# Kernel optimization log

Hardware: AMD Instinct MI355X
Metric: run time of the kernel (lower is better)

The kernel has to match this reference:

```python
import jax, jax.numpy as jnp
import numpy as np

L, D, DM, H, FF = 2048, 32, 1024, 16, 4096
DH = DM // H  # 64
SCALE = float(np.sqrt(DH))


def layernorm(x, g, b, eps=1e-5):
    mu = jnp.mean(x, axis=-1, keepdims=True)
    var = jnp.mean(jnp.square(x - mu), axis=-1, keepdims=True)
    return (x - mu) * jax.lax.rsqrt(var + eps) * g + b


def setup_inputs() -> dict:
    key = jax.random.key(0)
    ks = jax.random.split(key, 8)
    p = lambda k, shp: jax.random.normal(k, shp, jnp.float32) * 0.02
    return {
        "src": jax.random.normal(ks[0], (L, DM), jnp.float32),
        "target": jax.random.normal(ks[1], (L, D, DM), jnp.float32),
        "attn_mask": jnp.zeros((L, D), jnp.float32),
        "Wq": p(ks[2], (DM, DM)), "bq": jnp.zeros((DM,), jnp.float32),
        "Wk": p(ks[3], (DM, DM)), "bk": jnp.zeros((DM,), jnp.float32),
        "Wv": p(ks[4], (DM, DM)), "bv": jnp.zeros((DM,), jnp.float32),
        "W1": p(ks[5], (DM, FF)), "b1": jnp.zeros((FF,), jnp.float32),
        "W2": p(ks[6], (FF, DM)), "b2": jnp.zeros((DM,), jnp.float32),
        "g1": jnp.ones((DM,), jnp.float32), "beta1": jnp.zeros((DM,), jnp.float32),
        "g2": jnp.ones((DM,), jnp.float32), "beta2": jnp.zeros((DM,), jnp.float32),
    }


def reference(src, target, attn_mask, Wq, bq, Wk, bk, Wv, bv,
              W1, b1, W2, b2, g1, beta1, g2, beta2):
    # projections: src (L, DM), target (L, D, DM)
    q = (src @ Wq + bq).reshape(L, H, DH)            # (L, H, DH)
    k = (target @ Wk + bk).reshape(L, D, H, DH)       # (L, D, H, DH)
    v = (target @ Wv + bv).reshape(L, D, H, DH)
    # per-position attention over the D candidates: scores (H, L, D)
    scores = jnp.einsum('lhd,lkhd->hlk', q, k) / SCALE
    scores = scores + attn_mask[None, :, :]
    probs = jax.nn.softmax(scores, axis=-1)
    ctx = jnp.einsum('hlk,lkhd->lhd', probs, v).reshape(L, DM)
    x = layernorm(src + ctx, g1, beta1)
    ff = jax.nn.gelu(x @ W1 + b1, approximate=False) @ W2 + b2
    return layernorm(x + ff, g2, beta2)
```

## Files before the change

kernel.cpp:

```cpp
#include <hip/hip_runtime.h>
#include <hip/hip_bf16.h>

#define L  2048
#define D  32
#define DM 1024
#define H  16
#define DH 64
#define FF 4096

typedef unsigned short u16;
typedef __attribute__((ext_vector_type(8))) short bf16x8;
typedef __attribute__((ext_vector_type(4))) float f32x4;
typedef __attribute__((ext_vector_type(4))) unsigned int u32x4;
typedef __attribute__((ext_vector_type(8))) unsigned short u16x8;
typedef __attribute__((ext_vector_type(4))) unsigned short u16x4;

static __device__ __forceinline__ u16 f2bf(float f) {
    union { __hip_bfloat16 b; u16 u; } cv;
    cv.b = __float2bfloat16(f);
    return cv.u;
}
static __device__ __forceinline__ void gll16(const u16* gsrc, u16* ldst) {
    __builtin_amdgcn_global_load_lds(
        (const __attribute__((address_space(1))) unsigned int*)gsrc,
        (__attribute__((address_space(3))) unsigned int*)ldst, 16, 0, 0);
}

__global__ __launch_bounds__(256) void prep_all(
    const float* __restrict__ src, u16* __restrict__ osrc,
    const float* __restrict__ Wk,  u16* __restrict__ oWk,
    const float* __restrict__ Wq,  u16* __restrict__ oWq,
    const float* __restrict__ Wv,  u16* __restrict__ oWv,
    const float* __restrict__ W1,  u16* __restrict__ oW1,
    const float* __restrict__ W2,  u16* __restrict__ oW2)
{
    const int b = blockIdx.x, t = threadIdx.x;
    if (b >= 10240) {
        const int i = (b - 10240) * 256 + t;
        const int na4 = (L * DM) / 4;
        const float* in;  u16* out;  int j;
        if (i < na4) { in = src; out = osrc; j = i; }
        else         { in = Wk;  out = oWk;  j = i - na4; }
        const float4 v = reinterpret_cast<const float4*>(in)[j];
        u16x4 o = { f2bf(v.x), f2bf(v.y), f2bf(v.z), f2bf(v.w) };
        *reinterpret_cast<u16x4*>(out + (long)j * 4) = o;
        return;
    }
    __shared__ float tile[32][33];
    const float* in; u16* out; int R, C, bx, by;
    if (b < 1024)      { in = Wq; out = oWq; R = DM; C = DM; int bb = b;        bx = (bb & 31) * 32;  by = (bb >> 5) * 32; }
    else if (b < 2048) { in = Wv; out = oWv; R = DM; C = DM; int bb = b - 1024; bx = (bb & 31) * 32;  by = (bb >> 5) * 32; }
    else if (b < 6144) { in = W1; out = oW1; R = DM; C = FF; int bb = b - 2048; bx = (bb & 127) * 32; by = (bb >> 7) * 32; }
    else               { in = W2; out = oW2; R = FF; C = DM; int bb = b - 6144; bx = (bb & 31) * 32;  by = (bb >> 5) * 32; }
    const int tx = t & 31, ty = t >> 5;
    #pragma unroll
    for (int i = 0; i < 32; i += 8)
        tile[ty + i][tx] = in[(long)(by + ty + i) * C + bx + tx];
    __syncthreads();
    #pragma unroll
    for (int i = 0; i < 32; i += 8)
        out[(long)(bx + ty + i) * R + by + tx] = f2bf(tile[tx][ty + i]);
}

template<int EPI, int BN, int PIPE>
__global__ __launch_bounds__(256) void gemm128(
    const u16* __restrict__ A, int lda, long aZ,
    const u16* __restrict__ Bt, int ldb, long bZ,
    void* __restrict__ Cv, int ldc, long cZ,
    const float* __restrict__ bias, int biasZ, int K)
{
    constexpr int NI = BN / 32;
    constexpr int ASZ = 128 * 64, BSZ = BN * 64;
    __shared__ u16 As[(PIPE ? 2 : 1) * ASZ];
    __shared__ u16 Bs[(PIPE ? 2 : 1) * BSZ];
    const int t = threadIdx.x, lane = t & 63, w = t >> 6;
    const int z = blockIdx.z;
    const int nxy = gridDim.x * gridDim.y;
    int fid = blockIdx.y * gridDim.x + blockIdx.x;
    const int q8 = nxy >> 3;
    fid = (fid & 7) * q8 + (fid >> 3);
    const int bx = fid % gridDim.x, by = fid / gridDim.x;
    const int mBase = by * 128, nBase = bx * BN;
    const u16* Ab = A + (long)z * aZ;
    const u16* Bb = Bt + (long)z * bZ;
    const int wr = w >> 1, wc = w & 1;
    const int sr = lane >> 3, sg = lane & 7, sswz = sg ^ sr;
    f32x4 acc[4][NI];
    #pragma unroll
    for (int mi = 0; mi < 4; ++mi)
        #pragma unroll
        for (int ni = 0; ni < NI; ++ni) acc[mi][ni] = (f32x4){0.f, 0.f, 0.f, 0.f};

    auto STAGE = [&](int buf, int k0) {
        u16* Ad = As + buf * ASZ;
        u16* Bd = Bs + buf * BSZ;
        #pragma unroll
        for (int i = 0; i < 4; ++i) {
            const int r = w * 32 + i * 8 + sr;
            gll16(&Ab[(long)(mBase + r) * lda + k0 + sswz * 8], &Ad[r * 64 + sg * 8]);
        }
        #pragma unroll
        for (int i = 0; i < NI; ++i) {
            const int r = w * (BN / 4) + i * 8 + sr;
            gll16(&Bb[(long)(nBase + r) * ldb + k0 + sswz * 8], &Bd[r * 64 + sg * 8]);
        }
    };

    if (PIPE) { STAGE(0, 0); }
    int cur = 0;
    for (int k0 = 0; k0 < K; k0 += 64) {
        if (!PIPE) {
            STAGE(0, k0);
            __syncthreads();
        } else {
            __syncthreads();
            if (k0 + 64 < K) STAGE(cur ^ 1, k0 + 64);
        }
        const u16* Ar = As + cur * ASZ;
        const u16* Br = Bs + cur * BSZ;
        __builtin_amdgcn_s_setprio(1);
        #pragma unroll
        for (int ks = 0; ks < 2; ++ks) {
            bf16x8 aF[4], bF[NI];
            #pragma unroll
            for (int mi = 0; mi < 4; ++mi) {
                const int rr = wr * 64 + mi * 16 + (lane & 15);
                aF[mi] = *reinterpret_cast<const bf16x8*>(
                    &Ar[rr * 64 + ((ks * 4 + (lane >> 4)) ^ (rr & 7)) * 8]);
            }
            #pragma unroll
            for (int ni = 0; ni < NI; ++ni) {
                const int rr = wc * (BN / 2) + ni * 16 + (lane & 15);
                bF[ni] = *reinterpret_cast<const bf16x8*>(
                    &Br[rr * 64 + ((ks * 4 + (lane >> 4)) ^ (rr & 7)) * 8]);
            }
            #pragma unroll
            for (int mi = 0; mi < 4; ++mi)
                #pragma unroll
                for (int ni = 0; ni < NI; ++ni)
                    acc[mi][ni] = __builtin_amdgcn_mfma_f32_16x16x32_bf16(
                        aF[mi], bF[ni], acc[mi][ni], 0, 0, 0);
        }
        __builtin_amdgcn_s_setprio(0);
        if (!PIPE) __syncthreads();
        if (PIPE) cur ^= 1;
    }
    const int rb = mBase + wr * 64 + ((lane >> 4) << 2);
    const int cb = nBase + wc * (BN / 2) + (lane & 15);
    #pragma unroll
    for (int mi = 0; mi < 4; ++mi) {
        #pragma unroll
        for (int ni = 0; ni < NI; ++ni) {
            const int col = cb + ni * 16;
            const float badd = bias ? bias[(long)z * biasZ + col] : 0.f;
            #pragma unroll
            for (int i = 0; i < 4; ++i) {
                float v = acc[mi][ni][i] + badd;
                if (EPI == 2) v = 0.5f * v * (1.f + erff(v * 0.70710678118654752f));
                const long off = (long)z * cZ + (long)(rb + mi * 16 + i) * ldc + col;
                if (EPI == 1) reinterpret_cast<float*>(Cv)[off] = v;
                else          reinterpret_cast<u16*>(Cv)[off]  = f2bf(v);
            }
        }
    }
}

#define NLV5 8
__global__ __launch_bounds__(512, 2) void attn_v5(
    const u16* __restrict__ qk,
    const float* __restrict__ target,
    const float* __restrict__ mask,
    u16* __restrict__ tw)
{
    extern __shared__ u16 smem[];
    u16*   tgtS0 = smem;
    u16*   tgtS1 = smem + D * DM;
    f32x4* red   = (f32x4*)(smem + 2 * D * DM);

    const int t = threadIdx.x, lane = t & 63, w = t >> 6;
    const int g = lane >> 4, hm = lane & 15;
    const int l0 = blockIdx.x * NLV5;

    float4 pf[16];
    bf16x8 qc[2][4];
    {
        const float* tl = target + (long)l0 * (D * DM);
        #pragma unroll
        for (int it = 0; it < 16; ++it)
            pf[it] = reinterpret_cast<const float4*>(tl)[it * 512 + t];
        #pragma unroll
        for (int it = 0; it < 16; ++it) {
            const int i = it * 512 + t;
            const int d = i >> 8, mm = (i & 255) * 4, cc = mm ^ ((d & 15) << 3);
            u16x4 o = { f2bf(pf[it].x), f2bf(pf[it].y), f2bf(pf[it].z), f2bf(pf[it].w) };
            *reinterpret_cast<u16x4*>(&tgtS0[d * DM + cc]) = o;
        }
        const float* tn = target + (long)(l0 + 1) * (D * DM);
        #pragma unroll
        for (int it = 0; it < 16; ++it)
            pf[it] = reinterpret_cast<const float4*>(tn)[it * 512 + t];
        const u16* qb = qk + (long)l0 * (H * DM) + hm * DM + w * 128 + g * 8;
        #pragma unroll
        for (int ks = 0; ks < 4; ++ks)
            qc[0][ks] = *reinterpret_cast<const bf16x8*>(&qb[ks * 32]);
    }
    __syncthreads();

    #pragma unroll
    for (int li = 0; li < NLV5; ++li) {
        const int l = l0 + li;
        const int cur = li & 1, nxt = cur ^ 1;
        u16* curS = cur ? tgtS1 : tgtS0;
        u16* nxtS = cur ? tgtS0 : tgtS1;

        const float* mrow = mask + (long)l * D;
        float mk[8];
        #pragma unroll
        for (int r = 0; r < 4; ++r) { mk[r] = mrow[4 * g + r]; mk[4 + r] = mrow[16 + 4 * g + r]; }

        if (li < NLV5 - 1) {
            #pragma unroll
            for (int it = 0; it < 16; ++it) {
                const int i = it * 512 + t;
                const int d = i >> 8, mm = (i & 255) * 4, cc = mm ^ ((d & 15) << 3);
                u16x4 o = { f2bf(pf[it].x), f2bf(pf[it].y), f2bf(pf[it].z), f2bf(pf[it].w) };
                *reinterpret_cast<u16x4*>(&nxtS[d * DM + cc]) = o;
            }
            if (li < NLV5 - 2) {
                const float* tn = target + (long)(l + 2) * (D * DM);
                #pragma unroll
                for (int it = 0; it < 16; ++it)
                    pf[it] = reinterpret_cast<const float4*>(tn)[it * 512 + t];
            }
            const u16* qn = qk + (long)(l + 1) * (H * DM) + hm * DM + w * 128 + g * 8;
            #pragma unroll
            for (int ks = 0; ks < 4; ++ks)
                qc[nxt][ks] = *reinterpret_cast<const bf16x8*>(&qn[ks * 32]);
        }

        f32x4 a0 = {0.f, 0.f, 0.f, 0.f}, a1 = {0.f, 0.f, 0.f, 0.f};
        const int swz = hm << 3;
        #pragma unroll
        for (int ks = 0; ks < 4; ++ks) {
            const int mcol = w * 128 + ks * 32 + g * 8;
            const bf16x8 x0 = *reinterpret_cast<const bf16x8*>(&curS[hm * DM + (mcol ^ swz)]);
            const bf16x8 x1 = *reinterpret_cast<const bf16x8*>(&curS[(16 + hm) * DM + (mcol ^ swz)]);
            a0 = __builtin_amdgcn_mfma_f32_16x16x32_bf16(x0, qc[cur][ks], a0, 0, 0, 0);
            a1 = __builtin_amdgcn_mfma_f32_16x16x32_bf16(x1, qc[cur][ks], a1, 0, 0, 0);
        }
        red[(w * 2 + 0) * 64 + lane] = a0;
        red[(w * 2 + 1) * 64 + lane] = a1;
        __syncthreads();

        f32x4 s0 = red[lane], s1 = red[64 + lane];
        #pragma unroll
        for (int ww = 1; ww < 8; ++ww) {
            s0 += red[(ww * 2 + 0) * 64 + lane];
            s1 += red[(ww * 2 + 1) * 64 + lane];
        }

        float sc[8];
        #pragma unroll
        for (int r = 0; r < 4; ++r) {
            sc[r]     = s0[r] * 0.125f + mk[r];
            sc[4 + r] = s1[r] * 0.125f + mk[4 + r];
        }
        float mx = sc[0];
        #pragma unroll
        for (int r = 1; r < 8; ++r) mx = fmaxf(mx, sc[r]);
        mx = fmaxf(mx, __shfl_xor(mx, 16));
        mx = fmaxf(mx, __shfl_xor(mx, 32));
        float sum = 0.f;
        #pragma unroll
        for (int r = 0; r < 8; ++r) { sc[r] = __expf(sc[r] - mx); sum += sc[r]; }
        sum += __shfl_xor(sum, 16);
        sum += __shfl_xor(sum, 32);
        const float pinv = 1.0f / sum;
        bf16x8 pfrag;
        #pragma unroll
        for (int r = 0; r < 8; ++r) pfrag[r] = (short)f2bf(sc[r] * pinv);

        u16* twl = tw + (long)l * (H * DM);
        const f32x4 zero = {0.f, 0.f, 0.f, 0.f};
        #pragma unroll
        for (int i = 0; i < 8; ++i) {
            const int mg = w * 8 + i;
            const int m = mg * 16 + hm;
            bf16x8 af;
            #pragma unroll
            for (int j = 0; j < 4; ++j) {
                const int d0 = 4 * g + j;
                const int d1 = 16 + 4 * g + j;
                af[j]     = (short)curS[d0 * DM + (m ^ (d0 << 3))];
                af[4 + j] = (short)curS[d1 * DM + (m ^ (d0 << 3))];
            }
            const f32x4 c = __builtin_amdgcn_mfma_f32_16x16x32_bf16(af, pfrag, zero, 0, 0, 0);
            u16x4 o = { f2bf(c[0]), f2bf(c[1]), f2bf(c[2]), f2bf(c[3]) };
            *reinterpret_cast<u16x4*>(&twl[hm * DM + mg * 16 + 4 * g]) = o;
        }
        __syncthreads();
    }
}

__global__ __launch_bounds__(256) void ln_fuse(
    const float* __restrict__ a, const float* __restrict__ zb, int nz, long zstride,
    const float* __restrict__ bvec,
    const float* __restrict__ g, const float* __restrict__ be,
    float* __restrict__ o32, u16* __restrict__ o16)
{
    const int l = blockIdx.x, t = threadIdx.x;
    __shared__ float S[4], SS[4];
    __shared__ float stats[2];
    const float4 va = reinterpret_cast<const float4*>(a + (long)l * DM)[t];
    float v[4] = { va.x, va.y, va.z, va.w };
    for (int zi = 0; zi < nz; ++zi) {
        const float4 q = reinterpret_cast<const float4*>(zb + (long)zi * zstride + (long)l * DM)[t];
        v[0] += q.x; v[1] += q.y; v[2] += q.z; v[3] += q.w;
    }
    if (bvec) {
        const float4 vv = reinterpret_cast<const float4*>(bvec)[t];
        v[0] += vv.x; v[1] += vv.y; v[2] += vv.z; v[3] += vv.w;
    }
    float s  = v[0] + v[1] + v[2] + v[3];
    float ss = v[0]*v[0] + v[1]*v[1] + v[2]*v[2] + v[3]*v[3];
    #pragma unroll
    for (int off = 32; off; off >>= 1) { s += __shfl_down(s, off); ss += __shfl_down(ss, off); }
    if ((t & 63) == 0) { S[t >> 6] = s; SS[t >> 6] = ss; }
    __syncthreads();
    if (t == 0) {
        const float St  = S[0] + S[1] + S[2] + S[3];
        const float SSt = SS[0] + SS[1] + SS[2] + SS[3];
        const float mu  = St * (1.f / DM);
        const float var = fmaxf(SSt * (1.f / DM) - mu * mu, 0.f);
        stats[0] = mu;
        stats[1] = rsqrtf(var + 1e-5f);
    }
    __syncthreads();
    const float mu = stats[0], rs = stats[1];
    const int c0 = t * 4;
    float ov[4];
    #pragma unroll
    for (int j = 0; j < 4; ++j) ov[j] = (v[j] - mu) * rs * g[c0 + j] + be[c0 + j];
    float4 o; o.x = ov[0]; o.y = ov[1]; o.z = ov[2]; o.w = ov[3];
    reinterpret_cast<float4*>(o32 + (long)l * DM)[t] = o;
    if (o16) {
        u16x4 q = { f2bf(ov[0]), f2bf(ov[1]), f2bf(ov[2]), f2bf(ov[3]) };
        *reinterpret_cast<u16x4*>(o16 + (long)l * DM + c0) = q;
    }
}

extern "C" void kernel_launch(void* const* d_in, const int* in_sizes, int n_in,
                              void* d_out, int out_size, void* d_ws, size_t ws_size,
                              hipStream_t stream)
{
    const float* src    = (const float*)d_in[0];
    const float* target = (const float*)d_in[1];
    const float* amask  = (const float*)d_in[2];
    const float* Wq = (const float*)d_in[3];
    const float* bq = (const float*)d_in[4];
    const float* Wk = (const float*)d_in[5];
    const float* Wv = (const float*)d_in[7];
    const float* bv = (const float*)d_in[8];
    const float* W1 = (const float*)d_in[9];
    const float* b1 = (const float*)d_in[10];
    const float* W2 = (const float*)d_in[11];
    const float* b2 = (const float*)d_in[12];
    const float* g1  = (const float*)d_in[13];
    const float* be1 = (const float*)d_in[14];
    const float* g2  = (const float*)d_in[15];
    const float* be2 = (const float*)d_in[16];

    char* ws = (char*)d_ws;
    const size_t MB = (size_t)1 << 20;
    u16*   src16 = (u16*)  (ws +  0 * MB);
    u16*   Wk16  = (u16*)  (ws +  4 * MB);
    u16*   WqT   = (u16*)  (ws +  6 * MB);
    u16*   WvT   = (u16*)  (ws +  8 * MB);
    u16*   W1T   = (u16*)  (ws + 10 * MB);
    u16*   W2T   = (u16*)  (ws + 18 * MB);
    u16*   Q16   = (u16*)  (ws + 26 * MB);
    u16*   qk16  = (u16*)  (ws + 30 * MB);
    u16*   Y16   = (u16*)  (ws + 30 * MB);
    float* ctx32 = (float*)(ws + 54 * MB);
    float* x32   = (float*)(ws + 62 * MB);
    u16*   x16   = (u16*)  (ws + 70 * MB);
    u16*   tw16  = (u16*)  (ws + 94 * MB);
    float* Z32   = (float*)(ws + 94 * MB);

    prep_all<<<13312, 256, 0, stream>>>(src, src16, Wk, Wk16,
                                        Wq, WqT, Wv, WvT, W1, W1T, W2, W2T);

    gemm128<0, 64, 1><<<dim3(DM / 64, L / 128, 1), 256, 0, stream>>>(
        src16, DM, 0, WqT, DM, 0, Q16, DM, 0, bq, 0, DM);
    gemm128<0, 128, 0><<<dim3(DM / 128, L / 128, H), 256, 0, stream>>>(
        Q16, DM, DH, Wk16, DM, DH, qk16, H * DM, DM, nullptr, 0, DH);

    (void)hipFuncSetAttribute(reinterpret_cast<const void*>(&attn_v5),
                              hipFuncAttributeMaxDynamicSharedMemorySize, 144 * 1024);
    attn_v5<<<L / NLV5, 512, 144 * 1024, stream>>>(qk16, target, amask, tw16);

    gemm128<1, 64, 1><<<dim3(1, L / 128, H), 256, 0, stream>>>(
        tw16, H * DM, DM, WvT, DM, (long)DH * DM, ctx32, DM, DH, bv, DH, DM);
    ln_fuse<<<L, 256, 0, stream>>>(src, ctx32, 1, 0, nullptr, g1, be1, x32, x16);
    gemm128<2, 128, 1><<<dim3(FF / 128, L / 128, 1), 256, 0, stream>>>(
        x16, DM, 0, W1T, DM, 0, Y16, FF, 0, b1, 0, DM);
    gemm128<1, 128, 1><<<dim3(DM / 128, L / 128, 4), 256, 0, stream>>>(
        Y16, FF, 1024, W2T, FF, 1024, Z32, DM, (long)L * DM, nullptr, 0, 1024);
    ln_fuse<<<L, 256, 0, stream>>>(x32, Z32, 4, (long)L * DM, b2, g2, be2, (float*)d_out, nullptr);
}
```

Before: 242.7 us.

## Compute attention scores redundantly per wave to drop cross-wave LDS reduction

In the attention kernel, each wave now computes the full 1024-long score dot product itself. Before, each wave covered a 128-column slice and the partial scores were reduced through shared memory. This removes the reduction buffer, one barrier per position and the register double-buffering of q, which is now loaded directly from global memory inside the loop. The cost is eight times more score MFMAs and eight times more shared and global reads for the score phase, since every wave repeats the same work. Shared memory per block drops from 144 KB to 128 KB.

```diff
diff --git a/kernel.cpp b/kernel.cpp
--- a/kernel.cpp
+++ b/kernel.cpp
@@ -165,24 +165,19 @@
     }
 }
 
-#define NLV5 8
-__global__ __launch_bounds__(512, 2) void attn_v5(
+#define NLV6 8
+__global__ __launch_bounds__(512, 2) void attn_v6(
     const u16* __restrict__ qk,
     const float* __restrict__ target,
     const float* __restrict__ mask,
     u16* __restrict__ tw)
 {
     extern __shared__ u16 smem[];
-    u16*   tgtS0 = smem;
-    u16*   tgtS1 = smem + D * DM;
-    f32x4* red   = (f32x4*)(smem + 2 * D * DM);
-
     const int t = threadIdx.x, lane = t & 63, w = t >> 6;
     const int g = lane >> 4, hm = lane & 15;
-    const int l0 = blockIdx.x * NLV5;
+    const int l0 = blockIdx.x * NLV6;
 
     float4 pf[16];
-    bf16x8 qc[2][4];
     {
         const float* tl = target + (long)l0 * (D * DM);
         #pragma unroll
@@ -193,32 +188,22 @@
             const int i = it * 512 + t;
             const int d = i >> 8, mm = (i & 255) * 4, cc = mm ^ ((d & 15) << 3);
             u16x4 o = { f2bf(pf[it].x), f2bf(pf[it].y), f2bf(pf[it].z), f2bf(pf[it].w) };
-            *reinterpret_cast<u16x4*>(&tgtS0[d * DM + cc]) = o;
+            *reinterpret_cast<u16x4*>(&smem[d * DM + cc]) = o;
         }
         const float* tn = target + (long)(l0 + 1) * (D * DM);
         #pragma unroll
         for (int it = 0; it < 16; ++it)
             pf[it] = reinterpret_cast<const float4*>(tn)[it * 512 + t];
-        const u16* qb = qk + (long)l0 * (H * DM) + hm * DM + w * 128 + g * 8;
-        #pragma unroll
-        for (int ks = 0; ks < 4; ++ks)
-            qc[0][ks] = *reinterpret_cast<const bf16x8*>(&qb[ks * 32]);
-    }
-    __syncthreads();
-
-    #pragma unroll
-    for (int li = 0; li < NLV5; ++li) {
+    }
+
+    #pragma unroll
+    for (int li = 0; li < NLV6; ++li) {
         const int l = l0 + li;
-        const int cur = li & 1, nxt = cur ^ 1;
-        u16* curS = cur ? tgtS1 : tgtS0;
-        u16* nxtS = cur ? tgtS0 : tgtS1;
-
-        const float* mrow = mask + (long)l * D;
-        float mk[8];
-        #pragma unroll
-        for (int r = 0; r < 4; ++r) { mk[r] = mrow[4 * g + r]; mk[4 + r] = mrow[16 + 4 * g + r]; }
-
-        if (li < NLV5 - 1) {
+        u16* curS = (li & 1) ? smem + D * DM : smem;
+        u16* nxtS = (li & 1) ? smem : smem + D * DM;
+        __syncthreads();
+
+        if (li < NLV6 - 1) {
             #pragma unroll
             for (int it = 0; it < 16; ++it) {
                 const int i = it * 512 + t;
@@ -226,44 +211,37 @@
                 u16x4 o = { f2bf(pf[it].x), f2bf(pf[it].y), f2bf(pf[it].z), f2bf(pf[it].w) };
                 *reinterpret_cast<u16x4*>(&nxtS[d * DM + cc]) = o;
             }
-            if (li < NLV5 - 2) {
+            if (li < NLV6 - 2) {
                 const float* tn = target + (long)(l + 2) * (D * DM);
                 #pragma unroll
                 for (int it = 0; it < 16; ++it)
                     pf[it] = reinterpret_cast<const float4*>(tn)[it * 512 + t];
             }
-            const u16* qn = qk + (long)(l + 1) * (H * DM) + hm * DM + w * 128 + g * 8;
-            #pragma unroll
-            for (int ks = 0; ks < 4; ++ks)
-                qc[nxt][ks] = *reinterpret_cast<const bf16x8*>(&qn[ks * 32]);
-        }
-
-        f32x4 a0 = {0.f, 0.f, 0.f, 0.f}, a1 = {0.f, 0.f, 0.f, 0.f};
+        }
+
+        const float* mrow = mask + (long)l * D;
+        float mk[8];
+        #pragma unroll
+        for (int r = 0; r < 4; ++r) { mk[r] = mrow[4 * g + r]; mk[4 + r] = mrow[16 + 4 * g + r]; }
+
+        f32x4 acc0 = {0.f, 0.f, 0.f, 0.f}, acc1 = {0.f, 0.f, 0.f, 0.f};
+        const u16* qrow = qk + (long)l * (H * DM) + hm * DM;
         const int swz = hm << 3;
-        #pragma unroll
-        for (int ks = 0; ks < 4; ++ks) {
-            const int mcol = w * 128 + ks * 32 + g * 8;
+        #pragma unroll 4
+        for (int ks = 0; ks < 32; ++ks) {
+            const int mcol = ks * 32 + g * 8;
+            const bf16x8 yf = *reinterpret_cast<const bf16x8*>(&qrow[mcol]);
             const bf16x8 x0 = *reinterpret_cast<const bf16x8*>(&curS[hm * DM + (mcol ^ swz)]);
             const bf16x8 x1 = *reinterpret_cast<const bf16x8*>(&curS[(16 + hm) * DM + (mcol ^ swz)]);
-            a0 = __builtin_amdgcn_mfma_f32_16x16x32_bf16(x0, qc[cur][ks], a0, 0, 0, 0);
-            a1 = __builtin_amdgcn_mfma_f32_16x16x32_bf16(x1, qc[cur][ks], a1, 0, 0, 0);
-        }
-        red[(w * 2 + 0) * 64 + lane] = a0;
-        red[(w * 2 + 1) * 64 + lane] = a1;
-        __syncthreads();
-
-        f32x4 s0 = red[lane], s1 = red[64 + lane];
-        #pragma unroll
-        for (int ww = 1; ww < 8; ++ww) {
-            s0 += red[(ww * 2 + 0) * 64 + lane];
-            s1 += red[(ww * 2 + 1) * 64 + lane];
+            acc0 = __builtin_amdgcn_mfma_f32_16x16x32_bf16(x0, yf, acc0, 0, 0, 0);
+            acc1 = __builtin_amdgcn_mfma_f32_16x16x32_bf16(x1, yf, acc1, 0, 0, 0);
         }
 
         float sc[8];
         #pragma unroll
         for (int r = 0; r < 4; ++r) {
-            sc[r]     = s0[r] * 0.125f + mk[r];
-            sc[4 + r] = s1[r] * 0.125f + mk[4 + r];
+            sc[r]     = acc0[r] * 0.125f + mk[r];
+            sc[4 + r] = acc1[r] * 0.125f + mk[4 + r];
         }
         float mx = sc[0];
         #pragma unroll
@@ -298,7 +276,6 @@
             u16x4 o = { f2bf(c[0]), f2bf(c[1]), f2bf(c[2]), f2bf(c[3]) };
             *reinterpret_cast<u16x4*>(&twl[hm * DM + mg * 16 + 4 * g]) = o;
         }
-        __syncthreads();
     }
 }
 
@@ -395,9 +372,9 @@
     gemm128<0, 128, 0><<<dim3(DM / 128, L / 128, H), 256, 0, stream>>>(
         Q16, DM, DH, Wk16, DM, DH, qk16, H * DM, DM, nullptr, 0, DH);
 
-    (void)hipFuncSetAttribute(reinterpret_cast<const void*>(&attn_v5),
-                              hipFuncAttributeMaxDynamicSharedMemorySize, 144 * 1024);
-    attn_v5<<<L / NLV5, 512, 144 * 1024, stream>>>(qk16, target, amask, tw16);
+    (void)hipFuncSetAttribute(reinterpret_cast<const void*>(&attn_v6),
+                              hipFuncAttributeMaxDynamicSharedMemorySize, 128 * 1024);
+    attn_v6<<<L / NLV6, 512, 128 * 1024, stream>>>(qk16, target, amask, tw16);
 
     gemm128<1, 64, 1><<<dim3(1, L / 128, H), 256, 0, stream>>>(
         tw16, H * DM, DM, WvT, DM, (long)DH * DM, ctx32, DM, DH, bv, DH, DM);
```

Result: slower. 278.3 us (+14.7%).
